# Kernel tuning notes

Measured on AMD Instinct MI355X. Metric: run time of the kernel, lower is better.

The kernel has to match this reference:

```python
import jax, jax.numpy as jnp
import numpy as np

# dims matching init_kwargs
B, T, F = 512, 2048, 32
BULK, COH = 8, 8
OUT = 6
COH_SIZE, BULK_SIZE = COH * 2, BULK * 3

# Turon cohesive-law constants (bilinear traction-separation)
D0, DF = 0.01, 0.1          # onset / final effective opening
# J2 plasticity constants (plane-stress, linear isotropic hardening)
E_MOD, NU = 1000.0, 0.3
SIGY0, HARD = 10.0, 100.0
G_MOD = E_MOD / (2.0 * (1.0 + NU))
_c = E_MOD / (1.0 - NU ** 2)
D_NP = np.array([[_c, _c * NU, 0.0], [_c * NU, _c, 0.0], [0.0, 0.0, _c * (1.0 - NU) / 2.0]], dtype=np.float32)
DINV_NP = np.linalg.inv(D_NP).astype(np.float32)


def setup_inputs() -> dict:
    key = jax.random.key(0)
    k1, k2, k3, k4 = jax.random.split(key, 4)
    x = jax.random.normal(k1, (B, T, F), jnp.float32) * 0.05
    W11 = jax.random.normal(k2, (COH_SIZE, F), jnp.float32) / np.sqrt(F)
    W12 = jax.random.normal(k3, (BULK_SIZE, F), jnp.float32) / np.sqrt(F)
    W2 = jax.random.normal(k4, (OUT, BULK_SIZE), jnp.float32) / np.sqrt(BULK_SIZE)
    return {"x": x, "W11": W11, "W12": W12, "W2": W2}


def _forward(x, W11, W12, W2):
    Bb, Tt, _ = x.shape
    # tiny per-point linear layers, batched over (B, T) up front
    coh_in = jnp.einsum('btf,cf->btc', x, W11).reshape(Bb, Tt, COH, 2)    # separations
    bulk_in = jnp.einsum('btf,cf->btc', x, W12).reshape(Bb, Tt, BULK, 3)  # strains
    W2s = jax.nn.softplus(W2)  # softLayer: positivity-constrained weights
    D = jnp.asarray(D_NP)
    DINV = jnp.asarray(DINV_NP)

    def step(carry, inp):
        d_hist, eps_p, kappa = carry          # [B,COH], [B,BULK,3], [B,BULK]
        delta, eps = inp                      # [B,COH,2], [B,BULK,3]
        # --- Turon cohesive update: history = max damage; loading flag ---
        dn, ds = delta[..., 0], delta[..., 1]
        lam = jnp.sqrt(jnp.maximum(dn, 0.0) ** 2 + ds ** 2 + 1e-12)
        d_new = jnp.clip(DF * (lam - D0) / (lam * (DF - D0)), 0.0, 1.0)
        d = jnp.maximum(d_hist, d_new)
        loading = (d_new > d_hist).astype(eps.dtype)
        # (cohesive tractions are computed in the torch code but never consumed)
        # --- J2 plane-stress return mapping with linear hardening ---
        sig_tr = jnp.einsum('bpi,ji->bpj', eps - eps_p, D)
        sxx, syy, sxy = sig_tr[..., 0], sig_tr[..., 1], sig_tr[..., 2]
        seq = jnp.sqrt(sxx ** 2 - sxx * syy + syy ** 2 + 3.0 * sxy ** 2 + 1e-12)
        sigY = SIGY0 + HARD * kappa
        dk = jnp.maximum(seq - sigY, 0.0) / (3.0 * G_MOD + HARD)
        f = jnp.where(seq > sigY, (sigY + HARD * dk) / seq, 1.0)
        sig = f[..., None] * sig_tr
        eps_p_n = eps - jnp.einsum('bpj,ij->bpi', sig, DINV)
        kappa_n = kappa + dk
        # --- damage coupling: if not loading, degrade bulk stress by (1-d) ---
        dam_b = d[:, :BULK]
        load_b = loading[:, :BULK]
        sig = jnp.where((load_b == 0.0)[..., None], sig * (1.0 - dam_b)[..., None], sig)
        out_t = sig.reshape(Bb, BULK_SIZE) @ W2s.T  # [B,OUT]
        return (d, eps_p_n, kappa_n), out_t

    carry0 = (jnp.zeros((Bb, COH), x.dtype), jnp.zeros((Bb, BULK, 3), x.dtype), jnp.zeros((Bb, BULK), x.dtype))
    _, outs = jax.lax.scan(step, carry0, (coh_in.swapaxes(0, 1), bulk_in.swapaxes(0, 1)))
    return outs.swapaxes(0, 1)  # [B,T,OUT]


def reference(x, W11, W12, W2):
    return _forward(x, W11, W12, W2)
```

## Files before the change

kernel.cpp:

```cpp
#include <hip/hip_runtime.h>
#include <math.h>

static constexpr int BT  = 512;
static constexpr int TT  = 2048;

static constexpr float C00 = (float)(1000.0 / (1.0 - 0.09));
static constexpr float C01 = (float)((1000.0 / (1.0 - 0.09)) * 0.3);
static constexpr float C22 = (float)((1000.0 / (1.0 - 0.09)) * 0.35);
static constexpr float INV3GH = (float)(1.0 / (3.0 * (1000.0 / 2.6) + 100.0));
static constexpr float SQ3 = 1.7320508075688772f;
static constexpr float IR3 = 0.57735026918962576f;

typedef float f2 __attribute__((ext_vector_type(2)));

__device__ __forceinline__ float softplus_f(float v) {
    return fmaxf(v, 0.0f) + log1pf(expf(-fabsf(v)));
}

__device__ __forceinline__ void plastic_window(
    float e0, float e1, float e2, int lane,
    float& Pxx, float& Pyy, float& Pxy, float& sigY, float& sigY2,
    float& sxx, float& syy, float& sxy, float& f)
{
    sxx = e0 - Pxx; syy = e1 - Pyy; sxy = e2 - Pxy;
    float q = fmaf(sxy, sxy, 1e-12f);
    q = fmaf(syy, syy, q);
    q = fmaf(sxx, sxx - syy, q);
    f = 1.0f;
    unsigned long long mask = __ballot(q > sigY2);
    while (mask) {
        int ts = __ffsll((long long)mask) - 1;
        float qs  = __shfl(q, ts);
        float sxs = __shfl(sxx, ts);
        float sys = __shfl(syy, ts);
        float sps = __shfl(sxy, ts);
        float rq  = __builtin_amdgcn_rsqf(qs);
        float seq = qs * rq;
        float dk  = (seq - sigY) * INV3GH;
        float fn  = fmaf(100.f, dk, sigY);
        float fs  = fn * rq;
        float om  = 1.0f - fs;
        Pxx = fmaf(om, sxs, Pxx);
        Pyy = fmaf(om, sys, Pyy);
        Pxy = fmaf(om, sps, Pxy);
        sigY = fn; sigY2 = fn * fn;
        if (lane == ts) f = fs;
        bool redo = lane > ts;
        if (redo) {
            sxx = e0 - Pxx; syy = e1 - Pyy; sxy = e2 - Pxy;
            q = fmaf(sxy, sxy, 1e-12f);
            q = fmaf(syy, syy, q);
            q = fmaf(sxx, sxx - syy, q);
        }
        mask = __ballot(redo && (q > sigY2));
    }
}

__global__ __launch_bounds__(512) void k_fused(
    const float* __restrict__ x, const float* __restrict__ W11,
    const float* __restrict__ W12, const float* __restrict__ W2,
    float* __restrict__ out)
{
    __shared__ __align__(16) float w11s[16 * 36];
    __shared__ __align__(16) float w12d[24 * 36];
    __shared__ float w2s[144];
    __shared__ __align__(16) float xs[4][64 * 36];
    __shared__ float red[2][64 * 51];

    const int tid  = threadIdx.x;
    const int lane = tid & 63;
    const int wv   = tid >> 6;
    const int b    = blockIdx.x;

    if (tid < 512) w11s[(tid >> 5) * 36 + (tid & 31)] = W11[tid];
    if (tid < 256) {
        int i = tid + 512;
        w11s[(i >> 5) * 36 + (i & 31)] = W11[i];
    }
    for (int i = tid; i < 768; i += 512) {
        int r = i >> 5, fc = i & 31;
        int p = r / 3, j = r - p * 3;
        const float* wb = W12 + p * 96 + fc;
        float v;
        if (j == 0)      v = C00 * wb[0]  + C01 * wb[32];
        else if (j == 1) v = C01 * wb[0]  + C00 * wb[32];
        else             v = (C22 * wb[64]) * SQ3;
        w12d[r * 36 + fc] = v;
    }
    if (tid < 144) {
        float v = softplus_f(W2[tid]);
        if ((tid % 24) % 3 == 2) v *= IR3;
        w2s[tid] = v;
    }
    const float4* xg4 = (const float4*)x + (size_t)b * (TT * 8);
    {
        int t = tid >> 3, c = tid & 7;
        float4 v0 = xg4[tid];
        float4 v1 = xg4[512 + tid];
        *(float4*)&xs[0][t * 36 + 4 * c] = v0;
        *(float4*)&xs[1][t * 36 + 4 * c] = v1;
    }
    __syncthreads();

    float w2r0[6], w2r1[6], w2r2[6];
    #pragma unroll
    for (int k = 0; k < 6; ++k) {
        w2r0[k] = w2s[k * 24 + 3 * wv];
        w2r1[k] = w2s[k * 24 + 3 * wv + 1];
        w2r2[k] = w2s[k * 24 + 3 * wv + 2];
    }
    const float4* wa0 = (const float4*)(w11s + (2 * wv) * 36);
    const float4* wa1 = (const float4*)(w11s + (2 * wv + 1) * 36);
    const float4* wb0 = (const float4*)(w12d + (3 * wv) * 36);
    const float4* wb1 = (const float4*)(w12d + (3 * wv + 1) * 36);
    const float4* wb2 = (const float4*)(w12d + (3 * wv + 2) * 36);

    float Pxx = 0.f, Pyy = 0.f, Pxy = 0.f;
    float sigY = 10.f, sigY2 = 100.f, d0 = 0.f;

    for (int s = 0; s < 16; ++s) {
        const int w0 = 2 * s, w1 = w0 + 1;
        const bool have = (s < 15);
        float4 nv0, nv1;
        if (have) {
            nv0 = xg4[(w0 + 2) * 512 + tid];
            nv1 = xg4[(w1 + 2) * 512 + tid];
        }

        const float* xr0 = &xs[w0 & 3][lane * 36];
        const float* xr1 = &xs[w1 & 3][lane * 36];
        f2 dnA = {0,0}, dsA = {0,0}, e0A = {0,0}, e1A = {0,0}, e2A = {0,0};
        f2 dnB = {0,0}, dsB = {0,0}, e0B = {0,0}, e1B = {0,0}, e2B = {0,0};
        #pragma unroll
        for (int c = 0; c < 8; ++c) {
            float4 a0 = wa0[c], a1 = wa1[c];
            float4 b0 = wb0[c], b1 = wb1[c], b2 = wb2[c];
            float4 xf0 = *(const float4*)(xr0 + 4 * c);
            float4 xf1 = *(const float4*)(xr1 + 4 * c);
            f2 xlo0 = {xf0.x, xf0.y}, xhi0 = {xf0.z, xf0.w};
            f2 xlo1 = {xf1.x, xf1.y}, xhi1 = {xf1.z, xf1.w};
            f2 t0, t1;
            t0 = (f2){a0.x, a0.y}; t1 = (f2){a0.z, a0.w};
            dnA = xlo0 * t0 + dnA;  dnA = xhi0 * t1 + dnA;
            dnB = xlo1 * t0 + dnB;  dnB = xhi1 * t1 + dnB;
            t0 = (f2){a1.x, a1.y}; t1 = (f2){a1.z, a1.w};
            dsA = xlo0 * t0 + dsA;  dsA = xhi0 * t1 + dsA;
            dsB = xlo1 * t0 + dsB;  dsB = xhi1 * t1 + dsB;
            t0 = (f2){b0.x, b0.y}; t1 = (f2){b0.z, b0.w};
            e0A = xlo0 * t0 + e0A;  e0A = xhi0 * t1 + e0A;
            e0B = xlo1 * t0 + e0B;  e0B = xhi1 * t1 + e0B;
            t0 = (f2){b1.x, b1.y}; t1 = (f2){b1.z, b1.w};
            e1A = xlo0 * t0 + e1A;  e1A = xhi0 * t1 + e1A;
            e1B = xlo1 * t0 + e1B;  e1B = xhi1 * t1 + e1B;
            t0 = (f2){b2.x, b2.y}; t1 = (f2){b2.z, b2.w};
            e2A = xlo0 * t0 + e2A;  e2A = xhi0 * t1 + e2A;
            e2B = xlo1 * t0 + e2B;  e2B = xhi1 * t1 + e2B;
        }
        float dn0 = dnA.x + dnA.y, ds0 = dsA.x + dsA.y;
        float e00 = e0A.x + e0A.y, e10 = e1A.x + e1A.y, e20 = e2A.x + e2A.y;
        float dn1 = dnB.x + dnB.y, ds1 = dsB.x + dsB.y;
        float e01 = e0B.x + e0B.y, e11 = e1B.x + e1B.y, e21 = e2B.x + e2B.y;

        float dnp0  = fmaxf(dn0, 0.f);
        float lam0  = sqrtf(fmaf(dnp0, dnp0, fmaf(ds0, ds0, 1e-12f)));
        float dnew0 = (0.1f * (lam0 - 0.01f)) / (lam0 * 0.09f);
        dnew0 = fminf(fmaxf(dnew0, 0.f), 1.f);
        float dnp1  = fmaxf(dn1, 0.f);
        float lam1  = sqrtf(fmaf(dnp1, dnp1, fmaf(ds1, ds1, 1e-12f)));
        float dnew1 = (0.1f * (lam1 - 0.01f)) / (lam1 * 0.09f);
        dnew1 = fminf(fmaxf(dnew1, 0.f), 1.f);

        float m0 = dnew0, m1 = dnew1;
        #pragma unroll
        for (int off = 1; off < 64; off <<= 1) {
            float t0 = __shfl_up(m0, off);
            float t1 = __shfl_up(m1, off);
            if (lane >= off) { m0 = fmaxf(m0, t0); m1 = fmaxf(m1, t1); }
        }
        float de0 = __shfl_up(m0, 1);
        de0 = (lane == 0) ? d0 : fmaxf(d0, de0);
        bool loading0 = dnew0 > de0;
        float di0 = fmaxf(de0, dnew0);
        float d0a = fmaxf(d0, __shfl(m0, 63));
        float de1 = __shfl_up(m1, 1);
        de1 = (lane == 0) ? d0a : fmaxf(d0a, de1);
        bool loading1 = dnew1 > de1;
        float di1 = fmaxf(de1, dnew1);
        d0 = fmaxf(d0a, __shfl(m1, 63));

        float sxx0, syy0, sxy0, f0;
        plastic_window(e00, e10, e20, lane, Pxx, Pyy, Pxy, sigY, sigY2,
                       sxx0, syy0, sxy0, f0);
        float scale0 = loading0 ? f0 : f0 * (1.0f - di0);
        float o00 = scale0 * sxx0, o10 = scale0 * syy0, o20 = scale0 * sxy0;

        float sxx1, syy1, sxy1, f1;
        plastic_window(e01, e11, e21, lane, Pxx, Pyy, Pxy, sigY, sigY2,
                       sxx1, syy1, sxy1, f1);
        float scale1 = loading1 ? f1 : f1 * (1.0f - di1);
        float o01 = scale1 * sxx1, o11 = scale1 * syy1, o21 = scale1 * sxy1;

        #pragma unroll
        for (int k = 0; k < 6; ++k) {
            float c0 = fmaf(o00, w2r0[k], fmaf(o10, w2r1[k], o20 * w2r2[k]));
            float c1 = fmaf(o01, w2r0[k], fmaf(o11, w2r1[k], o21 * w2r2[k]));
            red[0][lane * 51 + k * 8 + wv] = c0;
            red[1][lane * 51 + k * 8 + wv] = c1;
        }
        __syncthreads();

        if (tid < 384) {
            int t = tid & 63, k = tid >> 6;
            const float* rp0 = &red[0][t * 51 + k * 8];
            float a0 = ((rp0[0] + rp0[1]) + (rp0[2] + rp0[3]))
                     + ((rp0[4] + rp0[5]) + (rp0[6] + rp0[7]));
            out[((size_t)b * TT + w0 * 64 + t) * 6 + k] = a0;
            const float* rp1 = &red[1][t * 51 + k * 8];
            float a1 = ((rp1[0] + rp1[1]) + (rp1[2] + rp1[3]))
                     + ((rp1[4] + rp1[5]) + (rp1[6] + rp1[7]));
            out[((size_t)b * TT + w1 * 64 + t) * 6 + k] = a1;
        }
        if (have) {
            int t = tid >> 3, c = tid & 7;
            *(float4*)&xs[(w0 + 2) & 3][t * 36 + 4 * c] = nv0;
            *(float4*)&xs[(w1 + 2) & 3][t * 36 + 4 * c] = nv1;
        }
        __syncthreads();
    }
}

extern "C" void kernel_launch(void* const* d_in, const int* in_sizes, int n_in,
                              void* d_out, int out_size, void* d_ws, size_t ws_size,
                              hipStream_t stream)
{
    const float* x   = (const float*)d_in[0];
    const float* W11 = (const float*)d_in[1];
    const float* W12 = (const float*)d_in[2];
    const float* W2  = (const float*)d_in[3];
    float* out = (float*)d_out;

    hipLaunchKernelGGL(k_fused, dim3(BT), dim3(512), 0, stream,
                       x, W11, W12, W2, out);
}
```

Baseline: 119.8 us.

## Read x directly from global and double-buffer reduction to drop one barrier

Removes the shared-memory staging ring for x: each wave now loads its 64 timesteps straight from global memory inside the projection loop, and all 8 waves read the same rows, relying on cache hits. The output reduction buffer is double-buffered so the reduce-and-store for window pair s-1 happens after pair s's partials are written, which cuts one __syncthreads per iteration. A tail block flushes the last pair. The trade-off is global-load latency sitting directly on the serial recurrence path, with no explicit prefetch, in exchange for fewer barriers and less LDS use.

```diff
diff --git a/kernel.cpp b/kernel.cpp
--- a/kernel.cpp
+++ b/kernel.cpp
@@ -64,8 +64,7 @@
     __shared__ __align__(16) float w11s[16 * 36];
     __shared__ __align__(16) float w12d[24 * 36];
     __shared__ float w2s[144];
-    __shared__ __align__(16) float xs[4][64 * 36];
-    __shared__ float red[2][64 * 51];
+    __shared__ float red[2][2][64 * 51];
 
     const int tid  = threadIdx.x;
     const int lane = tid & 63;
@@ -92,14 +91,6 @@
         if ((tid % 24) % 3 == 2) v *= IR3;
         w2s[tid] = v;
     }
-    const float4* xg4 = (const float4*)x + (size_t)b * (TT * 8);
-    {
-        int t = tid >> 3, c = tid & 7;
-        float4 v0 = xg4[tid];
-        float4 v1 = xg4[512 + tid];
-        *(float4*)&xs[0][t * 36 + 4 * c] = v0;
-        *(float4*)&xs[1][t * 36 + 4 * c] = v1;
-    }
     __syncthreads();
 
     float w2r0[6], w2r1[6], w2r2[6];
@@ -115,28 +106,24 @@
     const float4* wb1 = (const float4*)(w12d + (3 * wv + 1) * 36);
     const float4* wb2 = (const float4*)(w12d + (3 * wv + 2) * 36);
 
+    const float4* xg4 = (const float4*)x + (size_t)b * (TT * 8);
+
     float Pxx = 0.f, Pyy = 0.f, Pxy = 0.f;
     float sigY = 10.f, sigY2 = 100.f, d0 = 0.f;
 
     for (int s = 0; s < 16; ++s) {
         const int w0 = 2 * s, w1 = w0 + 1;
-        const bool have = (s < 15);
-        float4 nv0, nv1;
-        if (have) {
-            nv0 = xg4[(w0 + 2) * 512 + tid];
-            nv1 = xg4[(w1 + 2) * 512 + tid];
-        }
-
-        const float* xr0 = &xs[w0 & 3][lane * 36];
-        const float* xr1 = &xs[w1 & 3][lane * 36];
+
+        const float4* xr0 = xg4 + (size_t)(w0 * 64 + lane) * 8;
+        const float4* xr1 = xg4 + (size_t)(w1 * 64 + lane) * 8;
         f2 dnA = {0,0}, dsA = {0,0}, e0A = {0,0}, e1A = {0,0}, e2A = {0,0};
         f2 dnB = {0,0}, dsB = {0,0}, e0B = {0,0}, e1B = {0,0}, e2B = {0,0};
         #pragma unroll
         for (int c = 0; c < 8; ++c) {
+            float4 xf0 = xr0[c];
+            float4 xf1 = xr1[c];
             float4 a0 = wa0[c], a1 = wa1[c];
             float4 b0 = wb0[c], b1 = wb1[c], b2 = wb2[c];
-            float4 xf0 = *(const float4*)(xr0 + 4 * c);
-            float4 xf1 = *(const float4*)(xr1 + 4 * c);
             f2 xlo0 = {xf0.x, xf0.y}, xhi0 = {xf0.z, xf0.w};
             f2 xlo1 = {xf1.x, xf1.y}, xhi1 = {xf1.z, xf1.w};
             f2 t0, t1;
@@ -204,28 +191,35 @@
         for (int k = 0; k < 6; ++k) {
             float c0 = fmaf(o00, w2r0[k], fmaf(o10, w2r1[k], o20 * w2r2[k]));
             float c1 = fmaf(o01, w2r0[k], fmaf(o11, w2r1[k], o21 * w2r2[k]));
-            red[0][lane * 51 + k * 8 + wv] = c0;
-            red[1][lane * 51 + k * 8 + wv] = c1;
-        }
-        __syncthreads();
-
-        if (tid < 384) {
+            red[s & 1][0][lane * 51 + k * 8 + wv] = c0;
+            red[s & 1][1][lane * 51 + k * 8 + wv] = c1;
+        }
+
+        if (s > 0 && tid < 384) {
             int t = tid & 63, k = tid >> 6;
-            const float* rp0 = &red[0][t * 51 + k * 8];
+            int pp = (s - 1) & 1;
+            const float* rp0 = &red[pp][0][t * 51 + k * 8];
             float a0 = ((rp0[0] + rp0[1]) + (rp0[2] + rp0[3]))
                      + ((rp0[4] + rp0[5]) + (rp0[6] + rp0[7]));
-            out[((size_t)b * TT + w0 * 64 + t) * 6 + k] = a0;
-            const float* rp1 = &red[1][t * 51 + k * 8];
+            out[((size_t)b * TT + (w0 - 2) * 64 + t) * 6 + k] = a0;
+            const float* rp1 = &red[pp][1][t * 51 + k * 8];
             float a1 = ((rp1[0] + rp1[1]) + (rp1[2] + rp1[3]))
                      + ((rp1[4] + rp1[5]) + (rp1[6] + rp1[7]));
-            out[((size_t)b * TT + w1 * 64 + t) * 6 + k] = a1;
-        }
-        if (have) {
-            int t = tid >> 3, c = tid & 7;
-            *(float4*)&xs[(w0 + 2) & 3][t * 36 + 4 * c] = nv0;
-            *(float4*)&xs[(w1 + 2) & 3][t * 36 + 4 * c] = nv1;
+            out[((size_t)b * TT + (w1 - 2) * 64 + t) * 6 + k] = a1;
         }
         __syncthreads();
+    }
+
+    if (tid < 384) {
+        int t = tid & 63, k = tid >> 6;
+        const float* rp0 = &red[1][0][t * 51 + k * 8];
+        float a0 = ((rp0[0] + rp0[1]) + (rp0[2] + rp0[3]))
+                 + ((rp0[4] + rp0[5]) + (rp0[6] + rp0[7]));
+        out[((size_t)b * TT + 30 * 64 + t) * 6 + k] = a0;
+        const float* rp1 = &red[1][1][t * 51 + k * 8];
+        float a1 = ((rp1[0] + rp1[1]) + (rp1[2] + rp1[3]))
+                 + ((rp1[4] + rp1[5]) + (rp1[6] + rp1[7]));
+        out[((size_t)b * TT + 31 * 64 + t) * 6 + k] = a1;
     }
 }
 
```

Result: slower. 189.1 us (+57.9%).
